# Optimization experiments

Measured on AMD Instinct MI355X. Metric: run time of the kernel, lower is better.

The kernel has to match this reference:

```python
import jax, jax.numpy as jnp
import numpy as np

B, C, H, W, K = 32, 256, 56, 56, 4  # batch, channels, spatial, branch count (connections)
HID = 32  # ceil(max(C//8,1)/8)*8


def setup_inputs() -> dict:
    key = jax.random.key(0)
    ks = jax.random.split(key, 7)
    y = jax.random.normal(ks[0], (B, C, H, W), jnp.float32)
    x = jax.random.normal(ks[1], (K, B, C, H, W), jnp.float32)
    W1 = jax.random.normal(ks[2], (HID, C * (K + 1)), jnp.float32) * 0.02
    gamma = 1.0 + 0.1 * jax.random.normal(ks[3], (HID,), jnp.float32)
    beta = 0.1 * jax.random.normal(ks[4], (HID,), jnp.float32)
    W2 = jax.random.normal(ks[5], (C * (K + 1), HID), jnp.float32) * 0.05
    b2 = 0.01 * jax.random.normal(ks[6], (C * (K + 1),), jnp.float32)
    return {"y": y, "x": x, "W1": W1, "gamma": gamma, "beta": beta, "W2": W2, "b2": b2}


def reference(y, x, W1, gamma, beta, W2, b2):
    k = x.shape[0]
    b = y.shape[0]
    # global average pools (the v.mean(dim=(2,3)) / y.mean(dim=(2,3)) in torch)
    ym = y.mean(axis=(2, 3))            # [B, C]
    xm = x.mean(axis=(3, 4))            # [K, B, C]
    # GatedConcatenationFunction: blocks [y_mean, x1_mean, ..., xK_mean] along channels
    w_in = jnp.concatenate([ym[None], xm], axis=0)          # [K+1, B, C]
    w_in = jnp.transpose(w_in, (1, 0, 2)).reshape(b, -1)     # [B, (K+1)*C]
    # 1x1 conv -> BN (inference: running mean 0, var 1) -> ReLU -> 1x1 conv (bias)
    h = jax.nn.relu(w_in @ W1.T * gamma + beta)              # [B, HID]
    w = (h @ W2.T + b2).reshape(b, k + 1, -1)                # [B, K+1, C]
    w1 = jax.nn.sigmoid(w[:, 0])                             # [B, C]  gate on y
    w2 = jax.nn.softmax(w[:, 1:], axis=1)                    # [B, K, C] softmax over branches
    # GatedAmplificationFunction: weighted sum across branches
    z = jnp.einsum('bkc,kbchw->bchw', w2, x)                 # [B, C, H, W]
    return y * w1[:, :, None, None] + z
```

## Files before the change

kernel.cpp:

```cpp
#include <hip/hip_runtime.h>
#include <math.h>

typedef float f4 __attribute__((ext_vector_type(4)));

constexpr int Bn   = 32;
constexpr int Cn   = 256;
constexpr int Kn   = 4;
constexpr int HIDn = 32;
constexpr int HWn  = 56 * 56;
constexpr int HW4n = HWn / 4;
constexpr int CK1  = Cn * (Kn + 1);
constexpr int ROWS = (Kn + 1) * Bn * Cn;

__global__ __launch_bounds__(256) void pool_kernel(const float* __restrict__ y,
                                                   const float* __restrict__ x,
                                                   float* __restrict__ w_in) {
    int row  = blockIdx.x * 4 + (threadIdx.x >> 6);
    int lane = threadIdx.x & 63;
    if (row >= ROWS) return;

    int c  = row % Cn;
    int kb = row / Cn;
    int b  = kb % Bn;
    int k  = kb / Bn;

    float s = 0.f;
    if (k == 0) {
        const f4* s4 = reinterpret_cast<const f4*>(y + (size_t)(b * Cn + c) * HWn);
        for (int i = lane; i < HW4n; i += 64) {
            f4 v = s4[i];
            s += (v.x + v.y) + (v.z + v.w);
        }
    } else {
        const f4* s4 = reinterpret_cast<const f4*>(
            x + ((size_t)((k - 1) * Bn + b) * Cn + c) * HWn);
        for (int i = lane; i < HW4n; i += 64) {
            f4 v = __builtin_nontemporal_load(s4 + i);
            s += (v.x + v.y) + (v.z + v.w);
        }
    }

    #pragma unroll
    for (int off = 32; off > 0; off >>= 1) s += __shfl_xor(s, off, 64);

    if (lane == 0) w_in[b * CK1 + k * Cn + c] = s * (1.0f / (float)HWn);
}

__global__ __launch_bounds__(256) void mlp_kernel(const float* __restrict__ w_in,
                                                  const float* __restrict__ W1,
                                                  const float* __restrict__ gamma,
                                                  const float* __restrict__ beta,
                                                  const float* __restrict__ W2,
                                                  const float* __restrict__ b2,
                                                  float* __restrict__ gates) {
    int b = blockIdx.x;
    __shared__ float s_in[CK1];
    __shared__ float s_h[HIDn];
    __shared__ float s_w[CK1];

    for (int i = threadIdx.x; i < CK1; i += 256) s_in[i] = w_in[b * CK1 + i];
    __syncthreads();

    {
        int j   = threadIdx.x >> 3;
        int sub = threadIdx.x & 7;
        const float* w1row = W1 + j * CK1;
        float p = 0.f;
        for (int i = sub; i < CK1; i += 8) p += s_in[i] * w1row[i];
        p += __shfl_xor(p, 1);
        p += __shfl_xor(p, 2);
        p += __shfl_xor(p, 4);
        if (sub == 0) {
            float hv = p * gamma[j] + beta[j];
            s_h[j] = hv > 0.f ? hv : 0.f;
        }
    }
    __syncthreads();

    for (int o = threadIdx.x; o < CK1; o += 256) {
        const float* w2row = W2 + o * HIDn;
        float acc = b2[o];
        #pragma unroll
        for (int i = 0; i < HIDn; ++i) acc += s_h[i] * w2row[i];
        s_w[o] = acc;
    }
    __syncthreads();

    int c = threadIdx.x;
    float g0 = 1.f / (1.f + expf(-s_w[c]));
    float s1 = s_w[Cn + c], s2 = s_w[2 * Cn + c], s3 = s_w[3 * Cn + c], s4 = s_w[4 * Cn + c];
    float m  = fmaxf(fmaxf(s1, s2), fmaxf(s3, s4));
    float e1 = expf(s1 - m), e2 = expf(s2 - m), e3 = expf(s3 - m), e4 = expf(s4 - m);
    float inv = 1.f / (e1 + e2 + e3 + e4);
    float* g = gates + (size_t)b * (5 * Cn);
    g[c]          = g0;
    g[Cn + c]     = e1 * inv;
    g[2 * Cn + c] = e2 * inv;
    g[3 * Cn + c] = e3 * inv;
    g[4 * Cn + c] = e4 * inv;
}

__global__ __launch_bounds__(256) void apply_kernel(const float* __restrict__ y,
                                                    const float* __restrict__ x,
                                                    const float* __restrict__ gates,
                                                    float* __restrict__ out) {
    int bid = blockIdx.x;
    int c = bid % Cn;
    int b = bid / Cn;
    const float* g = gates + (size_t)b * (5 * Cn);
    float g0 = g[c];
    float g1 = g[Cn + c];
    float g2 = g[2 * Cn + c];
    float g3 = g[3 * Cn + c];
    float g4 = g[4 * Cn + c];

    size_t plane = (size_t)bid * HWn;
    size_t xstep = (size_t)Bn * Cn * HWn;
    const f4* y4  = reinterpret_cast<const f4*>(y + plane);
    const f4* x14 = reinterpret_cast<const f4*>(x + plane);
    const f4* x24 = reinterpret_cast<const f4*>(x + plane + xstep);
    const f4* x34 = reinterpret_cast<const f4*>(x + plane + 2 * xstep);
    const f4* x44 = reinterpret_cast<const f4*>(x + plane + 3 * xstep);
    f4* o4 = reinterpret_cast<f4*>(out + plane);

    for (int i = threadIdx.x; i < HW4n; i += 256) {
        f4 vy = y4[i];
        f4 v1 = __builtin_nontemporal_load(x14 + i);
        f4 v2 = __builtin_nontemporal_load(x24 + i);
        f4 v3 = __builtin_nontemporal_load(x34 + i);
        f4 v4 = __builtin_nontemporal_load(x44 + i);
        f4 r;
        r.x = vy.x * g0 + v1.x * g1 + v2.x * g2 + v3.x * g3 + v4.x * g4;
        r.y = vy.y * g0 + v1.y * g1 + v2.y * g2 + v3.y * g3 + v4.y * g4;
        r.z = vy.z * g0 + v1.z * g1 + v2.z * g2 + v3.z * g3 + v4.z * g4;
        r.w = vy.w * g0 + v1.w * g1 + v2.w * g2 + v3.w * g3 + v4.w * g4;
        __builtin_nontemporal_store(r, o4 + i);
    }
}

extern "C" void kernel_launch(void* const* d_in, const int* in_sizes, int n_in,
                              void* d_out, int out_size, void* d_ws, size_t ws_size,
                              hipStream_t stream) {
    const float* y     = (const float*)d_in[0];
    const float* x     = (const float*)d_in[1];
    const float* W1    = (const float*)d_in[2];
    const float* gamma = (const float*)d_in[3];
    const float* beta  = (const float*)d_in[4];
    const float* W2    = (const float*)d_in[5];
    const float* b2    = (const float*)d_in[6];
    float* out = (float*)d_out;

    float* w_in  = (float*)d_ws;
    float* gates = w_in + (size_t)Bn * CK1;

    pool_kernel<<<ROWS / 4, 256, 0, stream>>>(y, x, w_in);
    mlp_kernel<<<Bn, 256, 0, stream>>>(w_in, W1, gamma, beta, W2, b2, gates);
    apply_kernel<<<Bn * Cn, 256, 0, stream>>>(y, x, gates, out);
}
```

Before: 198.2 us.

## Reorder pool and apply passes to keep tail of x and y resident in cache

The pool kernel now streams x for batches 0-23 with nontemporal loads, then reads x for batches 24-31 and all of y with regular loads so they stay in the last-level cache. The apply kernel processes batches in reverse order, so the cached planes are consumed first and use regular loads. The aim is to cut HBM traffic for the second pass over x and y. Whether it pays off depends on the MI355X Infinity Cache holding roughly 100 MB of cached data, and the reversed order may change DRAM access patterns.

```diff
diff --git a/kernel.cpp b/kernel.cpp
--- a/kernel.cpp
+++ b/kernel.cpp
@@ -12,30 +12,55 @@
 constexpr int CK1  = Cn * (Kn + 1);
 constexpr int ROWS = (Kn + 1) * Bn * Cn;
 
+constexpr int STREAM_ROWS = 24 * Kn * Cn;
+constexpr int KEEP_X_ROWS = 8 * Kn * Cn;
+
 __global__ __launch_bounds__(256) void pool_kernel(const float* __restrict__ y,
                                                    const float* __restrict__ x,
                                                    float* __restrict__ w_in) {
-    int row  = blockIdx.x * 4 + (threadIdx.x >> 6);
+    int w    = blockIdx.x * 4 + (threadIdx.x >> 6);
     int lane = threadIdx.x & 63;
-    if (row >= ROWS) return;
-
-    int c  = row % Cn;
-    int kb = row / Cn;
-    int b  = kb % Bn;
-    int k  = kb / Bn;
-
+    if (w >= ROWS) return;
+
+    int b, k, c;
+    const float* src;
+    bool nt;
+    if (w < STREAM_ROWS) {
+        b = w >> 10;
+        int r  = w & 1023;
+        int br = r >> 8;
+        c = r & 255;
+        k = br + 1;
+        nt = true;
+        src = x + ((size_t)(br * Bn + b) * Cn + c) * HWn;
+    } else if (w < STREAM_ROWS + KEEP_X_ROWS) {
+        int w2 = w - STREAM_ROWS;
+        b = 24 + (w2 >> 10);
+        int r  = w2 & 1023;
+        int br = r >> 8;
+        c = r & 255;
+        k = br + 1;
+        nt = false;
+        src = x + ((size_t)(br * Bn + b) * Cn + c) * HWn;
+    } else {
+        int w3 = w - (STREAM_ROWS + KEEP_X_ROWS);
+        b = w3 >> 8;
+        c = w3 & 255;
+        k = 0;
+        nt = false;
+        src = y + (size_t)(b * Cn + c) * HWn;
+    }
+
+    const f4* s4 = reinterpret_cast<const f4*>(src);
     float s = 0.f;
-    if (k == 0) {
-        const f4* s4 = reinterpret_cast<const f4*>(y + (size_t)(b * Cn + c) * HWn);
+    if (nt) {
+        for (int i = lane; i < HW4n; i += 64) {
+            f4 v = __builtin_nontemporal_load(s4 + i);
+            s += (v.x + v.y) + (v.z + v.w);
+        }
+    } else {
         for (int i = lane; i < HW4n; i += 64) {
             f4 v = s4[i];
-            s += (v.x + v.y) + (v.z + v.w);
-        }
-    } else {
-        const f4* s4 = reinterpret_cast<const f4*>(
-            x + ((size_t)((k - 1) * Bn + b) * Cn + c) * HWn);
-        for (int i = lane; i < HW4n; i += 64) {
-            f4 v = __builtin_nontemporal_load(s4 + i);
             s += (v.x + v.y) + (v.z + v.w);
         }
     }
@@ -105,8 +130,8 @@
                                                     const float* __restrict__ gates,
                                                     float* __restrict__ out) {
     int bid = blockIdx.x;
-    int c = bid % Cn;
-    int b = bid / Cn;
+    int b = 31 - (bid >> 8);
+    int c = bid & 255;
     const float* g = gates + (size_t)b * (5 * Cn);
     float g0 = g[c];
     float g1 = g[Cn + c];
@@ -114,7 +139,7 @@
     float g3 = g[3 * Cn + c];
     float g4 = g[4 * Cn + c];
 
-    size_t plane = (size_t)bid * HWn;
+    size_t plane = (size_t)(b * Cn + c) * HWn;
     size_t xstep = (size_t)Bn * Cn * HWn;
     const f4* y4  = reinterpret_cast<const f4*>(y + plane);
     const f4* x14 = reinterpret_cast<const f4*>(x + plane);
@@ -123,18 +148,34 @@
     const f4* x44 = reinterpret_cast<const f4*>(x + plane + 3 * xstep);
     f4* o4 = reinterpret_cast<f4*>(out + plane);
 
-    for (int i = threadIdx.x; i < HW4n; i += 256) {
-        f4 vy = y4[i];
-        f4 v1 = __builtin_nontemporal_load(x14 + i);
-        f4 v2 = __builtin_nontemporal_load(x24 + i);
-        f4 v3 = __builtin_nontemporal_load(x34 + i);
-        f4 v4 = __builtin_nontemporal_load(x44 + i);
-        f4 r;
-        r.x = vy.x * g0 + v1.x * g1 + v2.x * g2 + v3.x * g3 + v4.x * g4;
-        r.y = vy.y * g0 + v1.y * g1 + v2.y * g2 + v3.y * g3 + v4.y * g4;
-        r.z = vy.z * g0 + v1.z * g1 + v2.z * g2 + v3.z * g3 + v4.z * g4;
-        r.w = vy.w * g0 + v1.w * g1 + v2.w * g2 + v3.w * g3 + v4.w * g4;
-        __builtin_nontemporal_store(r, o4 + i);
+    if (b >= 24) {
+        for (int i = threadIdx.x; i < HW4n; i += 256) {
+            f4 vy = y4[i];
+            f4 v1 = x14[i];
+            f4 v2 = x24[i];
+            f4 v3 = x34[i];
+            f4 v4 = x44[i];
+            f4 r;
+            r.x = vy.x * g0 + v1.x * g1 + v2.x * g2 + v3.x * g3 + v4.x * g4;
+            r.y = vy.y * g0 + v1.y * g1 + v2.y * g2 + v3.y * g3 + v4.y * g4;
+            r.z = vy.z * g0 + v1.z * g1 + v2.z * g2 + v3.z * g3 + v4.z * g4;
+            r.w = vy.w * g0 + v1.w * g1 + v2.w * g2 + v3.w * g3 + v4.w * g4;
+            __builtin_nontemporal_store(r, o4 + i);
+        }
+    } else {
+        for (int i = threadIdx.x; i < HW4n; i += 256) {
+            f4 vy = y4[i];
+            f4 v1 = __builtin_nontemporal_load(x14 + i);
+            f4 v2 = __builtin_nontemporal_load(x24 + i);
+            f4 v3 = __builtin_nontemporal_load(x34 + i);
+            f4 v4 = __builtin_nontemporal_load(x44 + i);
+            f4 r;
+            r.x = vy.x * g0 + v1.x * g1 + v2.x * g2 + v3.x * g3 + v4.x * g4;
+            r.y = vy.y * g0 + v1.y * g1 + v2.y * g2 + v3.y * g3 + v4.y * g4;
+            r.z = vy.z * g0 + v1.z * g1 + v2.z * g2 + v3.z * g3 + v4.z * g4;
+            r.w = vy.w * g0 + v1.w * g1 + v2.w * g2 + v3.w * g3 + v4.w * g4;
+            __builtin_nontemporal_store(r, o4 + i);
+        }
     }
 }
 
```

After: 195.3 us. Within noise of the previous version (-1.5%).

## Pipeline pool, MLP and apply over batch chunks in one fused kernel

Applied to the files above, without the earlier changes.

Merges the three kernels into one kernel that dispatches on block index. It is launched once per stage of a software pipeline over batch chunks of four: pooling of chunk s, the MLP of chunk s-1 and the apply of chunk s-2 run in the same launch. The aim is to shorten the distance between the pooling read and the apply read of the same planes, so the second read can hit in the large last-level cache instead of HBM. Pooling loads switch from nontemporal to normal loads to favour cache retention, and the apply's y load becomes nontemporal. The cost is ten launches instead of three, and the reuse depends on the working set per stage fitting in cache.

```diff
diff --git a/kernel.cpp b/kernel.cpp
--- a/kernel.cpp
+++ b/kernel.cpp
@@ -10,131 +10,135 @@
 constexpr int HWn  = 56 * 56;
 constexpr int HW4n = HWn / 4;
 constexpr int CK1  = Cn * (Kn + 1);
-constexpr int ROWS = (Kn + 1) * Bn * Cn;
 
-__global__ __launch_bounds__(256) void pool_kernel(const float* __restrict__ y,
-                                                   const float* __restrict__ x,
-                                                   float* __restrict__ w_in) {
-    int row  = blockIdx.x * 4 + (threadIdx.x >> 6);
-    int lane = threadIdx.x & 63;
-    if (row >= ROWS) return;
+constexpr int CB          = 4;
+constexpr int NCHUNK      = Bn / CB;
+constexpr int POOL_ROWS   = CB * (Kn + 1) * Cn;
+constexpr int POOL_BLOCKS = POOL_ROWS / 4;
+constexpr int APPLY_BLOCKS= CB * Cn;
 
-    int c  = row % Cn;
-    int kb = row / Cn;
-    int b  = kb % Bn;
-    int k  = kb / Bn;
+__global__ __launch_bounds__(256) void pa_kernel(
+    const float* __restrict__ y, const float* __restrict__ x,
+    const float* __restrict__ W1, const float* __restrict__ gamma,
+    const float* __restrict__ beta, const float* __restrict__ W2,
+    const float* __restrict__ bias2,
+    float* __restrict__ w_in, float* __restrict__ gates,
+    float* __restrict__ out,
+    int pool_chunk, int mlp_chunk, int apply_chunk)
+{
+    const int nmlp  = (mlp_chunk  >= 0) ? CB : 0;
+    const int npool = (pool_chunk >= 0) ? POOL_BLOCKS : 0;
+    const int bid   = blockIdx.x;
 
-    float s = 0.f;
-    if (k == 0) {
-        const f4* s4 = reinterpret_cast<const f4*>(y + (size_t)(b * Cn + c) * HWn);
+    if (bid < nmlp) {
+        const int b = mlp_chunk * CB + bid;
+        __shared__ float s_in[CK1];
+        __shared__ float s_h[HIDn];
+        for (int i = threadIdx.x; i < CK1; i += 256) s_in[i] = w_in[b * CK1 + i];
+        __syncthreads();
+        {
+            int j   = threadIdx.x >> 3;
+            int sub = threadIdx.x & 7;
+            const float* w1row = W1 + j * CK1;
+            float p = 0.f;
+            for (int i = sub; i < CK1; i += 8) p += s_in[i] * w1row[i];
+            p += __shfl_xor(p, 1);
+            p += __shfl_xor(p, 2);
+            p += __shfl_xor(p, 4);
+            if (sub == 0) {
+                float hv = p * gamma[j] + beta[j];
+                s_h[j] = hv > 0.f ? hv : 0.f;
+            }
+        }
+        __syncthreads();
+        const int c = threadIdx.x;
+        float wv[5];
+        #pragma unroll
+        for (int k2 = 0; k2 < 5; ++k2) {
+            const float* w2row = W2 + (size_t)(k2 * Cn + c) * HIDn;
+            float acc = bias2[k2 * Cn + c];
+            #pragma unroll
+            for (int i = 0; i < HIDn; ++i) acc += s_h[i] * w2row[i];
+            wv[k2] = acc;
+        }
+        float g0 = 1.f / (1.f + expf(-wv[0]));
+        float m  = fmaxf(fmaxf(wv[1], wv[2]), fmaxf(wv[3], wv[4]));
+        float e1 = expf(wv[1] - m), e2 = expf(wv[2] - m);
+        float e3 = expf(wv[3] - m), e4 = expf(wv[4] - m);
+        float inv = 1.f / (e1 + e2 + e3 + e4);
+        float* gg = gates + (size_t)b * (5 * Cn);
+        gg[c]          = g0;
+        gg[Cn + c]     = e1 * inv;
+        gg[2 * Cn + c] = e2 * inv;
+        gg[3 * Cn + c] = e3 * inv;
+        gg[4 * Cn + c] = e4 * inv;
+    } else if (bid < nmlp + npool) {
+        const int g    = pool_chunk;
+        const int row  = (bid - nmlp) * 4 + (threadIdx.x >> 6);
+        const int lane = threadIdx.x & 63;
+
+        int b, k, c;
+        const float* src;
+        if (row < CB * Kn * Cn) {
+            int lb = row >> 10;
+            int br = (row >> 8) & 3;
+            c = row & 255;
+            b = g * CB + lb;
+            k = br + 1;
+            src = x + ((size_t)(br * Bn + b) * Cn + c) * HWn;
+        } else {
+            int r2 = row - CB * Kn * Cn;
+            int lb = r2 >> 8;
+            c = r2 & 255;
+            b = g * CB + lb;
+            k = 0;
+            src = y + (size_t)(b * Cn + c) * HWn;
+        }
+
+        const f4* s4 = reinterpret_cast<const f4*>(src);
+        float s = 0.f;
         for (int i = lane; i < HW4n; i += 64) {
             f4 v = s4[i];
             s += (v.x + v.y) + (v.z + v.w);
         }
+        #pragma unroll
+        for (int off = 32; off > 0; off >>= 1) s += __shfl_xor(s, off, 64);
+        if (lane == 0) w_in[b * CK1 + k * Cn + c] = s * (1.0f / (float)HWn);
     } else {
-        const f4* s4 = reinterpret_cast<const f4*>(
-            x + ((size_t)((k - 1) * Bn + b) * Cn + c) * HWn);
-        for (int i = lane; i < HW4n; i += 64) {
-            f4 v = __builtin_nontemporal_load(s4 + i);
-            s += (v.x + v.y) + (v.z + v.w);
+        const int ab = bid - nmlp - npool;
+        const int lb = ab >> 8;
+        const int c  = ab & 255;
+        const int b  = apply_chunk * CB + lb;
+
+        const float* gg = gates + (size_t)b * (5 * Cn);
+        const float g0 = gg[c];
+        const float g1 = gg[Cn + c];
+        const float g2 = gg[2 * Cn + c];
+        const float g3 = gg[3 * Cn + c];
+        const float g4 = gg[4 * Cn + c];
+
+        const size_t plane = (size_t)(b * Cn + c) * HWn;
+        const size_t xstep = (size_t)Bn * Cn * HWn;
+        const f4* y4  = reinterpret_cast<const f4*>(y + plane);
+        const f4* x14 = reinterpret_cast<const f4*>(x + plane);
+        const f4* x24 = reinterpret_cast<const f4*>(x + plane + xstep);
+        const f4* x34 = reinterpret_cast<const f4*>(x + plane + 2 * xstep);
+        const f4* x44 = reinterpret_cast<const f4*>(x + plane + 3 * xstep);
+        f4* o4 = reinterpret_cast<f4*>(out + plane);
+
+        for (int i = threadIdx.x; i < HW4n; i += 256) {
+            f4 vy = __builtin_nontemporal_load(y4 + i);
+            f4 v1 = __builtin_nontemporal_load(x14 + i);
+            f4 v2 = __builtin_nontemporal_load(x24 + i);
+            f4 v3 = __builtin_nontemporal_load(x34 + i);
+            f4 v4 = __builtin_nontemporal_load(x44 + i);
+            f4 r;
+            r.x = vy.x * g0 + v1.x * g1 + v2.x * g2 + v3.x * g3 + v4.x * g4;
+            r.y = vy.y * g0 + v1.y * g1 + v2.y * g2 + v3.y * g3 + v4.y * g4;
+            r.z = vy.z * g0 + v1.z * g1 + v2.z * g2 + v3.z * g3 + v4.z * g4;
+            r.w = vy.w * g0 + v1.w * g1 + v2.w * g2 + v3.w * g3 + v4.w * g4;
+            __builtin_nontemporal_store(r, o4 + i);
         }
-    }
-
-    #pragma unroll
-    for (int off = 32; off > 0; off >>= 1) s += __shfl_xor(s, off, 64);
-
-    if (lane == 0) w_in[b * CK1 + k * Cn + c] = s * (1.0f / (float)HWn);
-}
-
-__global__ __launch_bounds__(256) void mlp_kernel(const float* __restrict__ w_in,
-                                                  const float* __restrict__ W1,
-                                                  const float* __restrict__ gamma,
-                                                  const float* __restrict__ beta,
-                                                  const float* __restrict__ W2,
-                                                  const float* __restrict__ b2,
-                                                  float* __restrict__ gates) {
-    int b = blockIdx.x;
-    __shared__ float s_in[CK1];
-    __shared__ float s_h[HIDn];
-    __shared__ float s_w[CK1];
-
-    for (int i = threadIdx.x; i < CK1; i += 256) s_in[i] = w_in[b * CK1 + i];
-    __syncthreads();
-
-    {
-        int j   = threadIdx.x >> 3;
-        int sub = threadIdx.x & 7;
-        const float* w1row = W1 + j * CK1;
-        float p = 0.f;
-        for (int i = sub; i < CK1; i += 8) p += s_in[i] * w1row[i];
-        p += __shfl_xor(p, 1);
-        p += __shfl_xor(p, 2);
-        p += __shfl_xor(p, 4);
-        if (sub == 0) {
-            float hv = p * gamma[j] + beta[j];
-            s_h[j] = hv > 0.f ? hv : 0.f;
-        }
-    }
-    __syncthreads();
-
-    for (int o = threadIdx.x; o < CK1; o += 256) {
-        const float* w2row = W2 + o * HIDn;
-        float acc = b2[o];
-        #pragma unroll
-        for (int i = 0; i < HIDn; ++i) acc += s_h[i] * w2row[i];
-        s_w[o] = acc;
-    }
-    __syncthreads();
-
-    int c = threadIdx.x;
-    float g0 = 1.f / (1.f + expf(-s_w[c]));
-    float s1 = s_w[Cn + c], s2 = s_w[2 * Cn + c], s3 = s_w[3 * Cn + c], s4 = s_w[4 * Cn + c];
-    float m  = fmaxf(fmaxf(s1, s2), fmaxf(s3, s4));
-    float e1 = expf(s1 - m), e2 = expf(s2 - m), e3 = expf(s3 - m), e4 = expf(s4 - m);
-    float inv = 1.f / (e1 + e2 + e3 + e4);
-    float* g = gates + (size_t)b * (5 * Cn);
-    g[c]          = g0;
-    g[Cn + c]     = e1 * inv;
-    g[2 * Cn + c] = e2 * inv;
-    g[3 * Cn + c] = e3 * inv;
-    g[4 * Cn + c] = e4 * inv;
-}
-
-__global__ __launch_bounds__(256) void apply_kernel(const float* __restrict__ y,
-                                                    const float* __restrict__ x,
-                                                    const float* __restrict__ gates,
-                                                    float* __restrict__ out) {
-    int bid = blockIdx.x;
-    int c = bid % Cn;
-    int b = bid / Cn;
-    const float* g = gates + (size_t)b * (5 * Cn);
-    float g0 = g[c];
-    float g1 = g[Cn + c];
-    float g2 = g[2 * Cn + c];
-    float g3 = g[3 * Cn + c];
-    float g4 = g[4 * Cn + c];
-
-    size_t plane = (size_t)bid * HWn;
-    size_t xstep = (size_t)Bn * Cn * HWn;
-    const f4* y4  = reinterpret_cast<const f4*>(y + plane);
-    const f4* x14 = reinterpret_cast<const f4*>(x + plane);
-    const f4* x24 = reinterpret_cast<const f4*>(x + plane + xstep);
-    const f4* x34 = reinterpret_cast<const f4*>(x + plane + 2 * xstep);
-    const f4* x44 = reinterpret_cast<const f4*>(x + plane + 3 * xstep);
-    f4* o4 = reinterpret_cast<f4*>(out + plane);
-
-    for (int i = threadIdx.x; i < HW4n; i += 256) {
-        f4 vy = y4[i];
-        f4 v1 = __builtin_nontemporal_load(x14 + i);
-        f4 v2 = __builtin_nontemporal_load(x24 + i);
-        f4 v3 = __builtin_nontemporal_load(x34 + i);
-        f4 v4 = __builtin_nontemporal_load(x44 + i);
-        f4 r;
-        r.x = vy.x * g0 + v1.x * g1 + v2.x * g2 + v3.x * g3 + v4.x * g4;
-        r.y = vy.y * g0 + v1.y * g1 + v2.y * g2 + v3.y * g3 + v4.y * g4;
-        r.z = vy.z * g0 + v1.z * g1 + v2.z * g2 + v3.z * g3 + v4.z * g4;
-        r.w = vy.w * g0 + v1.w * g1 + v2.w * g2 + v3.w * g3 + v4.w * g4;
-        __builtin_nontemporal_store(r, o4 + i);
     }
 }
 
@@ -153,7 +157,13 @@
     float* w_in  = (float*)d_ws;
     float* gates = w_in + (size_t)Bn * CK1;
 
-    pool_kernel<<<ROWS / 4, 256, 0, stream>>>(y, x, w_in);
-    mlp_kernel<<<Bn, 256, 0, stream>>>(w_in, W1, gamma, beta, W2, b2, gates);
-    apply_kernel<<<Bn * Cn, 256, 0, stream>>>(y, x, gates, out);
+    for (int s = 0; s < NCHUNK + 2; ++s) {
+        int pc = (s < NCHUNK) ? s : -1;
+        int mc = (s - 1 >= 0 && s - 1 < NCHUNK) ? (s - 1) : -1;
+        int ac = (s - 2 >= 0 && s - 2 < NCHUNK) ? (s - 2) : -1;
+        int nblocks = (mc >= 0 ? CB : 0) + (pc >= 0 ? POOL_BLOCKS : 0)
+                    + (ac >= 0 ? APPLY_BLOCKS : 0);
+        pa_kernel<<<nblocks, 256, 0, stream>>>(
+            y, x, W1, gamma, beta, W2, b2, w_in, gates, out, pc, mc, ac);
+    }
 }
```

After: 365.2 us. +84.3%, slower.
